# Optimization experiments

Measured on AMD Instinct MI355X. Metric: run time of the kernel, lower is better.

Reference implementation:

```python
import jax, jax.numpy as jnp
import numpy as np

ALPHA = 0.1        # self.alpha in the torch module
NUM_CLASSES = 10   # predict_acc hardcodes range(10)


def _sqdist(x, centers):
    # Faithful to sum((x - c)**2, -1) but computed via the gemm identity to
    # avoid materializing the (N, K, D) broadcast the torch code creates.
    x2 = jnp.sum(x * x, axis=1, keepdims=True)          # [N, 1]
    c2 = jnp.sum(centers * centers, axis=1)             # [K]
    d = x2 + c2[None, :] - 2.0 * (x @ centers.T)        # [N, K]
    return jnp.maximum(d, 0.0)                          # clamp fp round-off


def _predict_acc(distance, y):
    n = distance.shape[0]
    y_p = jnp.argmin(distance, axis=1)                  # index[1][:, 0]
    # counts[i, c] = #points assigned to cluster i (only i < 10 matter) with label c
    onehot_cluster = (y_p[:, None] == jnp.arange(NUM_CLASSES)[None, :]).astype(jnp.float32)  # [N, 10]
    onehot_label = (y[:, None] == jnp.arange(NUM_CLASSES)[None, :]).astype(jnp.float32)      # [N, 10]
    counts = onehot_cluster.T @ onehot_label            # [10, 10]
    used = jnp.zeros((NUM_CLASSES,), dtype=bool)
    correct = jnp.float32(0.0)
    for i in range(NUM_CLASSES):
        bin_i = counts[i]
        has_points = jnp.sum(bin_i) > 0                 # empty bincount -> 'continue'
        label = jnp.argmax(bin_i)                       # first max index, like where(bin==max)[0][0]
        # quchong: recursively zero already-used labels == argmax with used masked out
        masked = jnp.where(used, 0.0, bin_i)
        label = jnp.where(used[label], jnp.argmax(masked), label)
        correct = correct + jnp.where(has_points, bin_i[label], 0.0)
        used = jnp.where(has_points, used.at[label].set(True), used)
    return correct / jnp.float32(n)


def setup_inputs() -> dict:
    key = jax.random.key(0)
    kx, ky, kc = jax.random.split(key, 3)
    N, K, D = 262144, 256, 64
    x = jax.random.normal(kx, (N, D), dtype=jnp.float32)
    y = jax.random.randint(ky, (N,), 0, 10, dtype=jnp.int64)
    centers = jax.random.normal(kc, (K, D), dtype=jnp.float32)
    return {"x": x, "y": y, "centers": centers}


def reference(x, y, centers):
    distance = _sqdist(x, centers)                      # caldis, op='l2'
    # calwei: exp(-alpha*log(d+1)) then row-normalize
    we = jnp.exp(-ALPHA * jnp.log1p(distance))
    weight = we / jnp.sum(we, axis=1, keepdims=True)
    loss = jnp.sum(weight * distance)                   # calloss
    acc = _predict_acc(distance, y)
    return (loss, acc)
```

## Files before the change

### kernel.cpp

```cpp
#include <hip/hip_runtime.h>

#define ALPHA 0.1f
#define NUM_CLASSES 10

typedef __attribute__((ext_vector_type(8))) short bf16x8;
typedef __attribute__((ext_vector_type(4))) float f32x4;


__device__ __forceinline__ unsigned pack2(float a, float b) {
    return (__float_as_uint(b) & 0xFFFF0000u) | (__float_as_uint(a) >> 16);
}
__device__ __forceinline__ float truncbf(float a) {
    return __uint_as_float(__float_as_uint(a) & 0xFFFF0000u);
}

__global__ __launch_bounds__(512, 4) void dist_kernel(
    const float* __restrict__ x,
    const int*   __restrict__ y,
    const float* __restrict__ centers,
    float* __restrict__ loss_acc,
    unsigned int* __restrict__ counts,
    int NT)
{
    __shared__ __align__(16) char bstage[8 * 4 * 64 * 16];
    __shared__ float x2s[128];
    __shared__ float c2s[256];
    __shared__ float    comb_swe[8][128];
    __shared__ float    comb_swd[8][128];
    __shared__ unsigned comb_best[8][128];
    __shared__ unsigned counts_l[100];

    const int tid  = threadIdx.x;
    const int w    = tid >> 6;
    const int lane = tid & 63;
    const int q    = lane >> 4;
    const int r    = lane & 15;

    if (tid < 100) counts_l[tid] = 0u;

    if (tid < 256) {
        const float4* crow = (const float4*)(centers + tid * 64);
        float s = 0.f;
#pragma unroll
        for (int j = 0; j < 16; ++j) {
            float4 v = crow[j];
            s = fmaf(v.x, v.x, s); s = fmaf(v.y, v.y, s);
            s = fmaf(v.z, v.z, s); s = fmaf(v.w, v.w, s);
        }
        c2s[tid] = s;
    }

    bf16x8 af[2][4];
#pragma unroll
    for (int ct = 0; ct < 2; ++ct) {
        const int row = w * 32 + ct * 16 + r;
        const float4* C = (const float4*)(centers + (size_t)row * 64);
        float4 v0 = C[q * 2], v1 = C[q * 2 + 1];
        float4 v2 = C[8 + q * 2], v3 = C[9 + q * 2];
        float4 m0 = make_float4(-2.f * v0.x, -2.f * v0.y, -2.f * v0.z, -2.f * v0.w);
        float4 m1 = make_float4(-2.f * v1.x, -2.f * v1.y, -2.f * v1.z, -2.f * v1.w);
        float4 m2 = make_float4(-2.f * v2.x, -2.f * v2.y, -2.f * v2.z, -2.f * v2.w);
        float4 m3 = make_float4(-2.f * v3.x, -2.f * v3.y, -2.f * v3.z, -2.f * v3.w);
        union { bf16x8 v; unsigned u[4]; } h0, h1, l0, l1;
        h0.u[0] = pack2(m0.x, m0.y); h0.u[1] = pack2(m0.z, m0.w);
        h0.u[2] = pack2(m1.x, m1.y); h0.u[3] = pack2(m1.z, m1.w);
        h1.u[0] = pack2(m2.x, m2.y); h1.u[1] = pack2(m2.z, m2.w);
        h1.u[2] = pack2(m3.x, m3.y); h1.u[3] = pack2(m3.z, m3.w);
        l0.u[0] = pack2(m0.x - truncbf(m0.x), m0.y - truncbf(m0.y));
        l0.u[1] = pack2(m0.z - truncbf(m0.z), m0.w - truncbf(m0.w));
        l0.u[2] = pack2(m1.x - truncbf(m1.x), m1.y - truncbf(m1.y));
        l0.u[3] = pack2(m1.z - truncbf(m1.z), m1.w - truncbf(m1.w));
        l1.u[0] = pack2(m2.x - truncbf(m2.x), m2.y - truncbf(m2.y));
        l1.u[1] = pack2(m2.z - truncbf(m2.z), m2.w - truncbf(m2.w));
        l1.u[2] = pack2(m3.x - truncbf(m3.x), m3.y - truncbf(m3.y));
        l1.u[3] = pack2(m3.z - truncbf(m3.z), m3.w - truncbf(m3.w));
        af[ct][0] = h0.v; af[ct][1] = h1.v; af[ct][2] = l0.v; af[ct][3] = l1.v;
    }

    float4 pv0, pv1, pv2, pv3;
    {
        const int row = blockIdx.x * 128 + w * 16 + r;
        const float4* X = (const float4*)(x + (size_t)row * 64);
        pv0 = X[q * 2]; pv1 = X[q * 2 + 1];
        pv2 = X[8 + q * 2]; pv3 = X[9 + q * 2];
    }

    __syncthreads();

    float c2r1[2][4];
#pragma unroll
    for (int ct = 0; ct < 2; ++ct) {
        float4 v = *(const float4*)(c2s + w * 32 + ct * 16 + q * 4);
        c2r1[ct][0] = v.x + 1.f; c2r1[ct][1] = v.y + 1.f;
        c2r1[ct][2] = v.z + 1.f; c2r1[ct][3] = v.w + 1.f;
    }

    float loss_local = 0.f;

    for (int t = blockIdx.x; t < NT; t += gridDim.x) {
        int ylab = 0;
        if (tid < 128) ylab = y[t * 128 + tid];

        {
            float4 v0 = pv0, v1 = pv1, v2 = pv2, v3 = pv3;

            const int tn = t + gridDim.x;
            if (tn < NT) {
                const int row = tn * 128 + w * 16 + r;
                const float4* X = (const float4*)(x + (size_t)row * 64);
                pv0 = X[q * 2]; pv1 = X[q * 2 + 1];
                pv2 = X[8 + q * 2]; pv3 = X[9 + q * 2];
            }

            float p = v0.x * v0.x;
            p = fmaf(v0.y, v0.y, p); p = fmaf(v0.z, v0.z, p); p = fmaf(v0.w, v0.w, p);
            p = fmaf(v1.x, v1.x, p); p = fmaf(v1.y, v1.y, p); p = fmaf(v1.z, v1.z, p); p = fmaf(v1.w, v1.w, p);
            p = fmaf(v2.x, v2.x, p); p = fmaf(v2.y, v2.y, p); p = fmaf(v2.z, v2.z, p); p = fmaf(v2.w, v2.w, p);
            p = fmaf(v3.x, v3.x, p); p = fmaf(v3.y, v3.y, p); p = fmaf(v3.z, v3.z, p); p = fmaf(v3.w, v3.w, p);
            p += __shfl_xor(p, 16);
            p += __shfl_xor(p, 32);
            if (q == 0) x2s[w * 16 + r] = p;

            union { bf16x8 v; uint4 u4; unsigned u[4]; } h0, h1, l0, l1;
            h0.u[0] = pack2(v0.x, v0.y); h0.u[1] = pack2(v0.z, v0.w);
            h0.u[2] = pack2(v1.x, v1.y); h0.u[3] = pack2(v1.z, v1.w);
            h1.u[0] = pack2(v2.x, v2.y); h1.u[1] = pack2(v2.z, v2.w);
            h1.u[2] = pack2(v3.x, v3.y); h1.u[3] = pack2(v3.z, v3.w);
            l0.u[0] = pack2(v0.x - truncbf(v0.x), v0.y - truncbf(v0.y));
            l0.u[1] = pack2(v0.z - truncbf(v0.z), v0.w - truncbf(v0.w));
            l0.u[2] = pack2(v1.x - truncbf(v1.x), v1.y - truncbf(v1.y));
            l0.u[3] = pack2(v1.z - truncbf(v1.z), v1.w - truncbf(v1.w));
            l1.u[0] = pack2(v2.x - truncbf(v2.x), v2.y - truncbf(v2.y));
            l1.u[1] = pack2(v2.z - truncbf(v2.z), v2.w - truncbf(v2.w));
            l1.u[2] = pack2(v3.x - truncbf(v3.x), v3.y - truncbf(v3.y));
            l1.u[3] = pack2(v3.z - truncbf(v3.z), v3.w - truncbf(v3.w));
            *(uint4*)(bstage + (((w * 4 + 0) * 64 + lane) << 4)) = h0.u4;
            *(uint4*)(bstage + (((w * 4 + 1) * 64 + lane) << 4)) = h1.u4;
            *(uint4*)(bstage + (((w * 4 + 2) * 64 + lane) << 4)) = l0.u4;
            *(uint4*)(bstage + (((w * 4 + 3) * 64 + lane) << 4)) = l1.u4;
        }
        __syncthreads();

#pragma unroll
        for (int pt = 0; pt < 8; ++pt) {
            union { uint4 u4; bf16x8 v; } b0, b1, b2, b3;
            b0.u4 = *(const uint4*)(bstage + (((pt * 4 + 0) * 64 + lane) << 4));
            b1.u4 = *(const uint4*)(bstage + (((pt * 4 + 1) * 64 + lane) << 4));
            b2.u4 = *(const uint4*)(bstage + (((pt * 4 + 2) * 64 + lane) << 4));
            b3.u4 = *(const uint4*)(bstage + (((pt * 4 + 3) * 64 + lane) << 4));
            const float x2p = x2s[pt * 16 + r];

            f32x4 acc[2];
#pragma unroll
            for (int ct = 0; ct < 2; ++ct) {
                f32x4 a;
                a[0] = x2p + c2r1[ct][0]; a[1] = x2p + c2r1[ct][1];
                a[2] = x2p + c2r1[ct][2]; a[3] = x2p + c2r1[ct][3];
                a = __builtin_amdgcn_mfma_f32_16x16x32_bf16(af[ct][0], b0.v, a, 0, 0, 0);
                a = __builtin_amdgcn_mfma_f32_16x16x32_bf16(af[ct][1], b1.v, a, 0, 0, 0);
                a = __builtin_amdgcn_mfma_f32_16x16x32_bf16(af[ct][2], b0.v, a, 0, 0, 0);
                a = __builtin_amdgcn_mfma_f32_16x16x32_bf16(af[ct][3], b1.v, a, 0, 0, 0);
                a = __builtin_amdgcn_mfma_f32_16x16x32_bf16(af[ct][0], b2.v, a, 0, 0, 0);
                a = __builtin_amdgcn_mfma_f32_16x16x32_bf16(af[ct][1], b3.v, a, 0, 0, 0);
                acc[ct] = a;
            }

            float swe = 0.f, swdu = 0.f;
            unsigned best = 0xFFFFFFFFu;
#pragma unroll
            for (int ct = 0; ct < 2; ++ct) {
#pragma unroll
                for (int reg = 0; reg < 4; ++reg) {
                    const float u = acc[ct][reg];
                    const unsigned kid = (unsigned)(w * 32 + ct * 16 + q * 4 + reg);
                    best = min(best, (__float_as_uint(u) & 0xFFFFFF00u) | kid);
                    float wg = exp2f(-ALPHA * __log2f(u));
                    swe += wg;
                    swdu = fmaf(wg, u, swdu);
                }
            }
            swe += __shfl_xor(swe, 16); swe += __shfl_xor(swe, 32);
            swdu += __shfl_xor(swdu, 16); swdu += __shfl_xor(swdu, 32);
            best = min(best, (unsigned)__shfl_xor((int)best, 16));
            best = min(best, (unsigned)__shfl_xor((int)best, 32));
            if (q == 0) {
                comb_swe[w][pt * 16 + r]  = swe;
                comb_swd[w][pt * 16 + r]  = swdu;
                comb_best[w][pt * 16 + r] = best;
            }
        }
        __syncthreads();

        if (tid < 128) {
            float SWE = comb_swe[0][tid], SWD = comb_swd[0][tid];
            unsigned BEST = comb_best[0][tid];
#pragma unroll
            for (int g = 1; g < 8; ++g) {
                SWE += comb_swe[g][tid];
                SWD += comb_swd[g][tid];
                BEST = min(BEST, comb_best[g][tid]);
            }
            loss_local += SWD / SWE - 1.f;
            const unsigned bk = BEST & 0xFFu;
            if (bk < NUM_CLASSES) {
                atomicAdd(&counts_l[bk * NUM_CLASSES + ylab], 1u);
            }
        }
    }

    if (w < 2) {
        float v = loss_local;
#pragma unroll
        for (int o = 32; o > 0; o >>= 1) v += __shfl_down(v, o);
        if (lane == 0) atomicAdd(loss_acc, v);
    }

    __syncthreads();
    if (tid < 100) {
        const unsigned c = counts_l[tid];
        if (c) atomicAdd(&counts[tid], c);
    }
}


__global__ void finalize_kernel(
    const float* __restrict__ loss_acc,
    const unsigned int* __restrict__ counts,
    float* __restrict__ out,
    int N)
{
    if (threadIdx.x == 0 && blockIdx.x == 0) {
        float c[NUM_CLASSES][NUM_CLASSES];
        for (int i = 0; i < NUM_CLASSES; ++i)
            for (int j = 0; j < NUM_CLASSES; ++j)
                c[i][j] = (float)counts[i * NUM_CLASSES + j];

        bool used[NUM_CLASSES];
        for (int i = 0; i < NUM_CLASSES; ++i) used[i] = false;

        float correct = 0.f;
        for (int i = 0; i < NUM_CLASSES; ++i) {
            float rowsum = 0.f;
            for (int j = 0; j < NUM_CLASSES; ++j) rowsum += c[i][j];
            bool has_points = rowsum > 0.f;

            int label = 0;
            float mx = c[i][0];
            for (int j = 1; j < NUM_CLASSES; ++j)
                if (c[i][j] > mx) { mx = c[i][j]; label = j; }

            if (used[label]) {
                float mm = used[0] ? 0.f : c[i][0];
                int l2 = 0;
                for (int j = 1; j < NUM_CLASSES; ++j) {
                    float v = used[j] ? 0.f : c[i][j];
                    if (v > mm) { mm = v; l2 = j; }
                }
                label = l2;
            }

            if (has_points) {
                correct += c[i][label];
                used[label] = true;
            }
        }
        out[0] = loss_acc[0];
        out[1] = correct / (float)N;
    }
}


extern "C" void kernel_launch(void* const* d_in, const int* in_sizes, int n_in,
                              void* d_out, int out_size, void* d_ws, size_t ws_size,
                              hipStream_t stream)
{
    const float* x       = (const float*)d_in[0];
    const int*   y       = (const int*)d_in[1];
    const float* centers = (const float*)d_in[2];
    float* out = (float*)d_out;

    const int N  = in_sizes[0] / 64;
    const int NT = N / 128;

    float* loss          = (float*)d_ws;
    unsigned int* counts = (unsigned int*)((char*)d_ws + 4);

    hipMemsetAsync(d_ws, 0, 512, stream);

    int grid = 1024;
    if (grid > NT) grid = NT;
    dist_kernel<<<grid, 512, 0, stream>>>(x, y, centers, loss, counts, NT);

    finalize_kernel<<<1, 64, 0, stream>>>(loss, counts, out, N);
}
```

Before: 157.0 us.

## Split tile staging into two halves to overlap conversion with MFMA compute

The per-tile pipeline is split into two phases. Waves 0-3 stage their rows into a half-size LDS buffer, all waves compute on those, then waves 4-7 stage the second half and all waves compute again. This is meant to shrink the LDS staging buffer and stagger conversion work against MFMA compute, at the cost of an extra barrier per tile and duplicated code. The finalize kernel now loads the count matrix into shared memory with parallel threads before the single-thread greedy pass.

```diff
diff --git a/kernel.cpp b/kernel.cpp
--- a/kernel.cpp
+++ b/kernel.cpp
@@ -22,7 +22,7 @@
     unsigned int* __restrict__ counts,
     int NT)
 {
-    __shared__ __align__(16) char bstage[8 * 4 * 64 * 16];
+    __shared__ __align__(16) char bstage[4 * 4 * 64 * 16];
     __shared__ float x2s[128];
     __shared__ float c2s[256];
     __shared__ float    comb_swe[8][128];
@@ -100,11 +100,10 @@
     for (int t = blockIdx.x; t < NT; t += gridDim.x) {
         int ylab = 0;
         if (tid < 128) ylab = y[t * 128 + tid];
-
-        {
+        const int tn = t + gridDim.x;
+
+        if (w < 4) {
             float4 v0 = pv0, v1 = pv1, v2 = pv2, v3 = pv3;
-
-            const int tn = t + gridDim.x;
             if (tn < NT) {
                 const int row = tn * 128 + w * 16 + r;
                 const float4* X = (const float4*)(x + (size_t)row * 64);
@@ -142,7 +141,7 @@
         __syncthreads();
 
 #pragma unroll
-        for (int pt = 0; pt < 8; ++pt) {
+        for (int pt = 0; pt < 4; ++pt) {
             union { uint4 u4; bf16x8 v; } b0, b1, b2, b3;
             b0.u4 = *(const uint4*)(bstage + (((pt * 4 + 0) * 64 + lane) << 4));
             b1.u4 = *(const uint4*)(bstage + (((pt * 4 + 1) * 64 + lane) << 4));
@@ -191,6 +190,94 @@
         }
         __syncthreads();
 
+        if (w >= 4) {
+            float4 v0 = pv0, v1 = pv1, v2 = pv2, v3 = pv3;
+            if (tn < NT) {
+                const int row = tn * 128 + w * 16 + r;
+                const float4* X = (const float4*)(x + (size_t)row * 64);
+                pv0 = X[q * 2]; pv1 = X[q * 2 + 1];
+                pv2 = X[8 + q * 2]; pv3 = X[9 + q * 2];
+            }
+
+            float p = v0.x * v0.x;
+            p = fmaf(v0.y, v0.y, p); p = fmaf(v0.z, v0.z, p); p = fmaf(v0.w, v0.w, p);
+            p = fmaf(v1.x, v1.x, p); p = fmaf(v1.y, v1.y, p); p = fmaf(v1.z, v1.z, p); p = fmaf(v1.w, v1.w, p);
+            p = fmaf(v2.x, v2.x, p); p = fmaf(v2.y, v2.y, p); p = fmaf(v2.z, v2.z, p); p = fmaf(v2.w, v2.w, p);
+            p = fmaf(v3.x, v3.x, p); p = fmaf(v3.y, v3.y, p); p = fmaf(v3.z, v3.z, p); p = fmaf(v3.w, v3.w, p);
+            p += __shfl_xor(p, 16);
+            p += __shfl_xor(p, 32);
+            if (q == 0) x2s[w * 16 + r] = p;
+
+            union { bf16x8 v; uint4 u4; unsigned u[4]; } h0, h1, l0, l1;
+            h0.u[0] = pack2(v0.x, v0.y); h0.u[1] = pack2(v0.z, v0.w);
+            h0.u[2] = pack2(v1.x, v1.y); h0.u[3] = pack2(v1.z, v1.w);
+            h1.u[0] = pack2(v2.x, v2.y); h1.u[1] = pack2(v2.z, v2.w);
+            h1.u[2] = pack2(v3.x, v3.y); h1.u[3] = pack2(v3.z, v3.w);
+            l0.u[0] = pack2(v0.x - truncbf(v0.x), v0.y - truncbf(v0.y));
+            l0.u[1] = pack2(v0.z - truncbf(v0.z), v0.w - truncbf(v0.w));
+            l0.u[2] = pack2(v1.x - truncbf(v1.x), v1.y - truncbf(v1.y));
+            l0.u[3] = pack2(v1.z - truncbf(v1.z), v1.w - truncbf(v1.w));
+            l1.u[0] = pack2(v2.x - truncbf(v2.x), v2.y - truncbf(v2.y));
+            l1.u[1] = pack2(v2.z - truncbf(v2.z), v2.w - truncbf(v2.w));
+            l1.u[2] = pack2(v3.x - truncbf(v3.x), v3.y - truncbf(v3.y));
+            l1.u[3] = pack2(v3.z - truncbf(v3.z), v3.w - truncbf(v3.w));
+            *(uint4*)(bstage + ((((w - 4) * 4 + 0) * 64 + lane) << 4)) = h0.u4;
+            *(uint4*)(bstage + ((((w - 4) * 4 + 1) * 64 + lane) << 4)) = h1.u4;
+            *(uint4*)(bstage + ((((w - 4) * 4 + 2) * 64 + lane) << 4)) = l0.u4;
+            *(uint4*)(bstage + ((((w - 4) * 4 + 3) * 64 + lane) << 4)) = l1.u4;
+        }
+        __syncthreads();
+
+#pragma unroll
+        for (int pt = 0; pt < 4; ++pt) {
+            union { uint4 u4; bf16x8 v; } b0, b1, b2, b3;
+            b0.u4 = *(const uint4*)(bstage + (((pt * 4 + 0) * 64 + lane) << 4));
+            b1.u4 = *(const uint4*)(bstage + (((pt * 4 + 1) * 64 + lane) << 4));
+            b2.u4 = *(const uint4*)(bstage + (((pt * 4 + 2) * 64 + lane) << 4));
+            b3.u4 = *(const uint4*)(bstage + (((pt * 4 + 3) * 64 + lane) << 4));
+            const float x2p = x2s[64 + pt * 16 + r];
+
+            f32x4 acc[2];
+#pragma unroll
+            for (int ct = 0; ct < 2; ++ct) {
+                f32x4 a;
+                a[0] = x2p + c2r1[ct][0]; a[1] = x2p + c2r1[ct][1];
+                a[2] = x2p + c2r1[ct][2]; a[3] = x2p + c2r1[ct][3];
+                a = __builtin_amdgcn_mfma_f32_16x16x32_bf16(af[ct][0], b0.v, a, 0, 0, 0);
+                a = __builtin_amdgcn_mfma_f32_16x16x32_bf16(af[ct][1], b1.v, a, 0, 0, 0);
+                a = __builtin_amdgcn_mfma_f32_16x16x32_bf16(af[ct][2], b0.v, a, 0, 0, 0);
+                a = __builtin_amdgcn_mfma_f32_16x16x32_bf16(af[ct][3], b1.v, a, 0, 0, 0);
+                a = __builtin_amdgcn_mfma_f32_16x16x32_bf16(af[ct][0], b2.v, a, 0, 0, 0);
+                a = __builtin_amdgcn_mfma_f32_16x16x32_bf16(af[ct][1], b3.v, a, 0, 0, 0);
+                acc[ct] = a;
+            }
+
+            float swe = 0.f, swdu = 0.f;
+            unsigned best = 0xFFFFFFFFu;
+#pragma unroll
+            for (int ct = 0; ct < 2; ++ct) {
+#pragma unroll
+                for (int reg = 0; reg < 4; ++reg) {
+                    const float u = acc[ct][reg];
+                    const unsigned kid = (unsigned)(w * 32 + ct * 16 + q * 4 + reg);
+                    best = min(best, (__float_as_uint(u) & 0xFFFFFF00u) | kid);
+                    float wg = exp2f(-ALPHA * __log2f(u));
+                    swe += wg;
+                    swdu = fmaf(wg, u, swdu);
+                }
+            }
+            swe += __shfl_xor(swe, 16); swe += __shfl_xor(swe, 32);
+            swdu += __shfl_xor(swdu, 16); swdu += __shfl_xor(swdu, 32);
+            best = min(best, (unsigned)__shfl_xor((int)best, 16));
+            best = min(best, (unsigned)__shfl_xor((int)best, 32));
+            if (q == 0) {
+                comb_swe[w][64 + pt * 16 + r]  = swe;
+                comb_swd[w][64 + pt * 16 + r]  = swdu;
+                comb_best[w][64 + pt * 16 + r] = best;
+            }
+        }
+        __syncthreads();
+
         if (tid < 128) {
             float SWE = comb_swe[0][tid], SWD = comb_swd[0][tid];
             unsigned BEST = comb_best[0][tid];
@@ -229,42 +316,44 @@
     float* __restrict__ out,
     int N)
 {
-    if (threadIdx.x == 0 && blockIdx.x == 0) {
-        float c[NUM_CLASSES][NUM_CLASSES];
-        for (int i = 0; i < NUM_CLASSES; ++i)
-            for (int j = 0; j < NUM_CLASSES; ++j)
-                c[i][j] = (float)counts[i * NUM_CLASSES + j];
-
+    __shared__ float cs[NUM_CLASSES * NUM_CLASSES];
+    __shared__ float ls;
+    const int tid = threadIdx.x;
+    if (tid < NUM_CLASSES * NUM_CLASSES) cs[tid] = (float)counts[tid];
+    if (tid == NUM_CLASSES * NUM_CLASSES) ls = loss_acc[0];
+    __syncthreads();
+    if (tid == 0) {
         bool used[NUM_CLASSES];
         for (int i = 0; i < NUM_CLASSES; ++i) used[i] = false;
 
         float correct = 0.f;
         for (int i = 0; i < NUM_CLASSES; ++i) {
+            const float* ci = cs + i * NUM_CLASSES;
             float rowsum = 0.f;
-            for (int j = 0; j < NUM_CLASSES; ++j) rowsum += c[i][j];
+            for (int j = 0; j < NUM_CLASSES; ++j) rowsum += ci[j];
             bool has_points = rowsum > 0.f;
 
             int label = 0;
-            float mx = c[i][0];
+            float mx = ci[0];
             for (int j = 1; j < NUM_CLASSES; ++j)
-                if (c[i][j] > mx) { mx = c[i][j]; label = j; }
+                if (ci[j] > mx) { mx = ci[j]; label = j; }
 
             if (used[label]) {
-                float mm = used[0] ? 0.f : c[i][0];
+                float mm = used[0] ? 0.f : ci[0];
                 int l2 = 0;
                 for (int j = 1; j < NUM_CLASSES; ++j) {
-                    float v = used[j] ? 0.f : c[i][j];
+                    float v = used[j] ? 0.f : ci[j];
                     if (v > mm) { mm = v; l2 = j; }
                 }
                 label = l2;
             }
 
             if (has_points) {
-                correct += c[i][label];
+                correct += ci[label];
                 used[label] = true;
             }
         }
-        out[0] = loss_acc[0];
+        out[0] = ls;
         out[1] = correct / (float)N;
     }
 }
@@ -291,5 +380,5 @@
     if (grid > NT) grid = NT;
     dist_kernel<<<grid, 512, 0, stream>>>(x, y, centers, loss, counts, NT);
 
-    finalize_kernel<<<1, 64, 0, stream>>>(loss, counts, out, N);
-}
+    finalize_kernel<<<1, 128, 0, stream>>>(loss, counts, out, N);
+}
```

Measured after the change: 150.5 us. 1.04x faster.
